# Kernel tuning notes

Measured on AMD Instinct MI355X. Metric: run time of the kernel, lower is better.

The kernel has to match this reference:

```python
import jax, jax.numpy as jnp
import numpy as np

N, E, D, L = 50000, 400000, 128, 5
NTYPE, NATTR, NDEPTH = 100, 100, 21
BN_EPS = 1e-5


def _bn(z, gamma, beta):
    # training-mode BatchNorm1d over the node axis (biased variance, as torch)
    mu = jnp.mean(z, axis=0)
    var = jnp.mean(jnp.square(z - mu), axis=0)
    return (z - mu) * jax.lax.rsqrt(var + BN_EPS) * gamma + beta


def setup_inputs() -> dict:
    key = jax.random.key(0)
    ks = jax.random.split(key, 20)
    s = 0.05
    inp = {
        "x": jax.random.randint(ks[0], (N, 2), 0, NTYPE),
        "node_depth": jax.random.randint(ks[1], (N,), 0, NDEPTH),
        "edge_index": jax.random.randint(ks[2], (2, E), 0, N),
        "edge_attr": jax.random.normal(ks[3], (E, 2), dtype=jnp.float32),
        # node encoder tables
        "type_emb": jax.random.normal(ks[4], (NTYPE, D)) * s,
        "attr_emb": jax.random.normal(ks[5], (NATTR, D)) * s,
        "depth_emb": jax.random.normal(ks[6], (NDEPTH, D)) * s,
        # per-layer GIN params, stacked over L
        "We": jax.random.normal(ks[7], (L, 2, D)) * s,
        "be": jnp.zeros((L, D)),
        "eps": jnp.zeros((L,)),
        "W1": jax.random.normal(ks[8], (L, D, 2 * D)) * s,
        "b1": jnp.zeros((L, 2 * D)),
        "g1": jnp.ones((L, 2 * D)),
        "bt1": jnp.zeros((L, 2 * D)),
        "W2": jax.random.normal(ks[9], (L, 2 * D, D)) * s,
        "b2": jnp.zeros((L, D)),
        "go": jnp.ones((L, D)),
        "bo": jnp.zeros((L, D)),
    }
    return inp


def reference(x, node_depth, edge_index, edge_attr,
              type_emb, attr_emb, depth_emb,
              We, be, eps, W1, b1, g1, bt1, W2, b2, go, bo):
    # node encoder: type + attr + depth embeddings  -> [N, D]
    h = (type_emb[x[:, 0]] + attr_emb[x[:, 1]]
         + depth_emb[jnp.clip(node_depth, 0, NDEPTH - 1)])
    src, dst = edge_index[0], edge_index[1]
    n = h.shape[0]
    for l in range(L):
        # GINConv: gather -> relu(x_j + edge_emb) -> scatter-add
        edge_emb = edge_attr @ We[l] + be[l]                 # [E, D]
        msg = jax.nn.relu(h[src] + edge_emb)                 # [E, D]
        agg = jax.ops.segment_sum(msg, dst, num_segments=n)  # [N, D]
        z = (1.0 + eps[l]) * h + agg
        # mlp: Linear -> BN -> ReLU -> Linear
        z = _bn(z @ W1[l] + b1[l], g1[l], bt1[l])
        z = jax.nn.relu(z) @ W2[l] + b2[l]
        # outer batchnorm
        z = _bn(z, go[l], bo[l])
        if l < L - 1:  # relu on all but last layer (dropout p=0 -> identity)
            z = jax.nn.relu(z)
        h = z
    return h  # JK='last'
```

## Files before the change

### kernel.cpp

```cpp
#include <hip/hip_runtime.h>
#include <hip/hip_bf16.h>

#define NN  50000
#define NE  400000
#define DD  128
#define DD2 256
#define NL  5
#define NB_SCAN 196
#define GB  256
#define NCH 1563

typedef __hip_bfloat16 bf16;
typedef __attribute__((ext_vector_type(8))) short bf16x8;
typedef __attribute__((ext_vector_type(4))) float f32x4;

__device__ __forceinline__ float b2f(bf16 v) { return __bfloat162float(v); }
__device__ __forceinline__ bool probe_bf(const void* g1) {
    return ((const unsigned*)g1)[0] == 0x3F803F80u;
}
__device__ __forceinline__ float ldp(const void* p, int i, bool bf) {
    return bf ? b2f(((const bf16*)p)[i]) : ((const float*)p)[i];
}
__device__ __forceinline__ void ldp8(const void* p, int i, bool bf, float* o) {
    if (bf) {
        union { int4 v; bf16 b[8]; } u;
        u.v = *(const int4*)((const bf16*)p + i);
#pragma unroll
        for (int j = 0; j < 8; j++) o[j] = b2f(u.b[j]);
    } else {
        float4 a = *(const float4*)((const float*)p + i);
        float4 b = *(const float4*)((const float*)p + i + 4);
        o[0]=a.x; o[1]=a.y; o[2]=a.z; o[3]=a.w;
        o[4]=b.x; o[5]=b.y; o[6]=b.z; o[7]=b.w;
    }
}

__global__ void enc_kernel(const int* __restrict__ x, const int* __restrict__ dep,
                           const void* te, const void* ae, const void* de,
                           const void* probe, float* __restrict__ h,
                           bf16* __restrict__ h2, int h2ok) {
    int t = blockIdx.x * 256 + threadIdx.x;
    if (t >= NN * DD) return;
    bool bf = probe_bf(probe);
    int i = t >> 7, d = t & (DD - 1);
    int dp = dep[i];
    dp = dp < 0 ? 0 : (dp > 20 ? 20 : dp);
    float a = ldp(te, x[2 * i] * DD + d, bf);
    float b = ldp(ae, x[2 * i + 1] * DD + d, bf);
    float c = ldp(de, dp * DD + d, bf);
    float s;
    if (bf) {
        s = b2f(__float2bfloat16(a + b));
        s = b2f(__float2bfloat16(s + c));
    } else {
        s = a + b + c;
    }
    h[t] = s;
    if (h2ok) h2[t] = __float2bfloat16(s);
}

__global__ void hist_kernel(const int* __restrict__ ei, int* __restrict__ cnt) {
    int e = blockIdx.x * 256 + threadIdx.x;
    if (e < NE) atomicAdd(&cnt[ei[NE + e]], 1);
}

__global__ void bsum_kernel(const int* __restrict__ cnt, int* __restrict__ bsum) {
    __shared__ int sm[256];
    int i = blockIdx.x * 256 + threadIdx.x;
    sm[threadIdx.x] = (i < NN) ? cnt[i] : 0;
    __syncthreads();
    for (int s = 128; s > 0; s >>= 1) {
        if (threadIdx.x < s) sm[threadIdx.x] += sm[threadIdx.x + s];
        __syncthreads();
    }
    if (threadIdx.x == 0) bsum[blockIdx.x] = sm[0];
}

__global__ void bscan_kernel(const int* __restrict__ bsum, int* __restrict__ boff, int nb) {
    __shared__ int sm[256];
    int t = threadIdx.x;
    int v = (t < nb) ? bsum[t] : 0;
    sm[t] = v; __syncthreads();
    for (int s = 1; s < 256; s <<= 1) {
        int a = (t >= s) ? sm[t - s] : 0;
        __syncthreads();
        sm[t] += a;
        __syncthreads();
    }
    if (t < nb) boff[t] = sm[t] - v;
}

__global__ void offs_kernel(const int* __restrict__ cnt, const int* __restrict__ boff,
                            int* __restrict__ offs, int* __restrict__ cur) {
    __shared__ int sm[256];
    int t = threadIdx.x;
    int i = blockIdx.x * 256 + t;
    int v = (i < NN) ? cnt[i] : 0;
    sm[t] = v; __syncthreads();
    for (int s = 1; s < 256; s <<= 1) {
        int a = (t >= s) ? sm[t - s] : 0;
        __syncthreads();
        sm[t] += a;
        __syncthreads();
    }
    int excl = sm[t] - v + boff[blockIdx.x];
    if (i < NN) { offs[i] = excl; cur[i] = excl; }
    if (i == NN - 1) offs[NN] = excl + v;
}

__global__ void place_kernel(const int* __restrict__ ei, const float* __restrict__ ea,
                             int* __restrict__ cur, int* __restrict__ srcS,
                             unsigned* __restrict__ eaS) {
    int e = blockIdx.x * 256 + threadIdx.x;
    if (e >= NE) return;
    int dst = ei[NE + e];
    int p = atomicAdd(&cur[dst], 1);
    srcS[p] = ei[e];
    union { bf16 b[2]; unsigned u; } pk;
    pk.b[0] = __float2bfloat16(ea[2 * e]);
    pk.b[1] = __float2bfloat16(ea[2 * e + 1]);
    eaS[p] = pk.u;
}

__global__ void wtrans2_kernel(const void* W1, const void* W2, const void* probe,
                               bf16* __restrict__ W1tH, bf16* __restrict__ W1tL,
                               bf16* __restrict__ W2tH, bf16* __restrict__ W2tL) {
    bool bf = probe_bf(probe);
    int idx = blockIdx.x * 256 + threadIdx.x;
    if (idx >= NL * DD * DD2) return;
    int l = idx / (DD * DD2), rem = idx % (DD * DD2);
    {
        int k = rem / DD2, n = rem % DD2;
        float w = ldp(W1, idx, bf);
        bf16 hb = __float2bfloat16(w);
        size_t o = ((size_t)l * DD2 + n) * DD + k;
        W1tH[o] = hb;
        W1tL[o] = __float2bfloat16(w - b2f(hb));
    }
    {
        int k = rem / DD, n = rem % DD;
        float w = ldp(W2, idx, bf);
        bf16 hb = __float2bfloat16(w);
        size_t o = ((size_t)l * DD + n) * DD2 + k;
        W2tH[o] = hb;
        W2tL[o] = __float2bfloat16(w - b2f(hb));
    }
}

template<int H2>
__global__ __launch_bounds__(256)
void agg_v2(const int* __restrict__ offs, const int* __restrict__ srcS,
            const unsigned* __restrict__ eaS, const void* We, const void* be,
            const void* epsp, const void* probe, const float* __restrict__ h,
            const bf16* __restrict__ h2, float* __restrict__ zpre, int l) {
    bool bf = probe_bf(probe);
    int wave = threadIdx.x >> 6, lane = threadIdx.x & 63;
    int node = blockIdx.x * 4 + wave;
    if (node >= NN) return;
    int d0 = lane * 2;
    float w00 = ldp(We, l * 2 * DD + d0, bf),      w01 = ldp(We, l * 2 * DD + d0 + 1, bf);
    float w10 = ldp(We, l * 2 * DD + DD + d0, bf), w11 = ldp(We, l * 2 * DD + DD + d0 + 1, bf);
    float bb0 = ldp(be, l * DD + d0, bf),          bb1 = ldp(be, l * DD + d0 + 1, bf);
    float cf = 1.0f + ldp(epsp, l, bf);
    int s = offs[node], e = offs[node + 1];
    float acc0 = 0.f, acc1 = 0.f;
    int j = s;
#define AGG_ONE(SRC, EA)                                                        \
    {   float hx, hy;                                                          \
        if (H2) { union { unsigned u; bf16 b[2]; } hv;                         \
                  hv.u = *(const unsigned*)&h2[(size_t)(SRC) * DD + d0];       \
                  hx = b2f(hv.b[0]); hy = b2f(hv.b[1]); }                      \
        else    { float2 hv = *(const float2*)&h[(size_t)(SRC) * DD + d0];     \
                  hx = hv.x; hy = hv.y; }                                      \
        union { unsigned u; bf16 b[2]; } ap; ap.u = (EA);                      \
        float ax = b2f(ap.b[0]), ay = b2f(ap.b[1]);                            \
        acc0 += fmaxf(hx + ax * w00 + ay * w10 + bb0, 0.f);                    \
        acc1 += fmaxf(hy + ax * w01 + ay * w11 + bb1, 0.f); }
    for (; j + 8 <= e; j += 8) {
        int i0=srcS[j],i1=srcS[j+1],i2=srcS[j+2],i3=srcS[j+3];
        int i4=srcS[j+4],i5=srcS[j+5],i6=srcS[j+6],i7=srcS[j+7];
        unsigned e0=eaS[j],e1=eaS[j+1],e2=eaS[j+2],e3=eaS[j+3];
        unsigned e4=eaS[j+4],e5=eaS[j+5],e6=eaS[j+6],e7=eaS[j+7];
        AGG_ONE(i0,e0) AGG_ONE(i1,e1) AGG_ONE(i2,e2) AGG_ONE(i3,e3)
        AGG_ONE(i4,e4) AGG_ONE(i5,e5) AGG_ONE(i6,e6) AGG_ONE(i7,e7)
    }
    for (; j + 4 <= e; j += 4) {
        int i0=srcS[j],i1=srcS[j+1],i2=srcS[j+2],i3=srcS[j+3];
        unsigned e0=eaS[j],e1=eaS[j+1],e2=eaS[j+2],e3=eaS[j+3];
        AGG_ONE(i0,e0) AGG_ONE(i1,e1) AGG_ONE(i2,e2) AGG_ONE(i3,e3)
    }
    for (; j < e; j++) { int i0 = srcS[j]; unsigned e0 = eaS[j]; AGG_ONE(i0,e0) }
#undef AGG_ONE
    float2 hs = *(const float2*)&h[(size_t)node * DD + d0];
    float2 o; o.x = fmaf(cf, hs.x, acc0); o.y = fmaf(cf, hs.y, acc1);
    *(float2*)&zpre[(size_t)node * DD + d0] = o;
}

__global__ __launch_bounds__(512, 2)
void gemm1_v2(const float* __restrict__ zpre, const bf16* __restrict__ W1tH,
              const bf16* __restrict__ W1tL, const void* b1, const void* probe,
              bf16* __restrict__ z1, float* __restrict__ P1s, float* __restrict__ P1q,
              int l) {
    __shared__ float smS[DD2], smQ[DD2];
    bool bf = probe_bf(probe);
    int tid = threadIdx.x;
    int lane = tid & 63, wave = tid >> 6;
    int wq = wave & 3, wr = wave >> 2;
    int ln15 = lane & 15, kg = lane >> 4;

    const bf16* WlH = W1tH + (size_t)l * DD2 * DD;
    const bf16* WlL = W1tL + (size_t)l * DD2 * DD;

    bf16x8 bh[4][4], bl[4][4];
#pragma unroll
    for (int t = 0; t < 4; t++) {
        int n = (wq * 4 + t) * 16 + ln15;
#pragma unroll
        for (int s = 0; s < 4; s++) {
            size_t off = (size_t)n * DD + s * 32 + kg * 8;
            bh[t][s] = *(const bf16x8*)&WlH[off];
            bl[t][s] = *(const bf16x8*)&WlL[off];
        }
    }
    float bias[4];
#pragma unroll
    for (int t = 0; t < 4; t++) bias[t] = ldp(b1, l * DD2 + (wq * 4 + t) * 16 + ln15, bf);

    float sp[4] = {0.f, 0.f, 0.f, 0.f}, qp[4] = {0.f, 0.f, 0.f, 0.f};

    for (int chunk = blockIdx.x; chunk < NCH; chunk += GB) {
        int rowbase = chunk * 32 + wr * 16;
        int arow = rowbase + ln15;
        bool aval = arow < NN;
        f32x4 acc[4];
#pragma unroll
        for (int t = 0; t < 4; t++) acc[t] = (f32x4){0.f, 0.f, 0.f, 0.f};
#pragma unroll
        for (int s = 0; s < 4; s++) {
            float av[8];
            if (aval) {
                float4 p0 = *(const float4*)&zpre[(size_t)arow * DD + s * 32 + kg * 8];
                float4 p1 = *(const float4*)&zpre[(size_t)arow * DD + s * 32 + kg * 8 + 4];
                av[0]=p0.x; av[1]=p0.y; av[2]=p0.z; av[3]=p0.w;
                av[4]=p1.x; av[5]=p1.y; av[6]=p1.z; av[7]=p1.w;
            } else {
#pragma unroll
                for (int j = 0; j < 8; j++) av[j] = 0.f;
            }
            union { bf16x8 v; bf16 e[8]; } ahi, alo;
#pragma unroll
            for (int j = 0; j < 8; j++) {
                bf16 hb = __float2bfloat16(av[j]);
                ahi.e[j] = hb;
                alo.e[j] = __float2bfloat16(av[j] - b2f(hb));
            }
#pragma unroll
            for (int t = 0; t < 4; t++) {
                acc[t] = __builtin_amdgcn_mfma_f32_16x16x32_bf16(ahi.v, bh[t][s], acc[t], 0, 0, 0);
                acc[t] = __builtin_amdgcn_mfma_f32_16x16x32_bf16(alo.v, bh[t][s], acc[t], 0, 0, 0);
                acc[t] = __builtin_amdgcn_mfma_f32_16x16x32_bf16(ahi.v, bl[t][s], acc[t], 0, 0, 0);
            }
        }
#pragma unroll
        for (int t = 0; t < 4; t++) {
            int col = (wq * 4 + t) * 16 + ln15;
#pragma unroll
            for (int r = 0; r < 4; r++) {
                int row = rowbase + kg * 4 + r;
                if (row < NN) {
                    float zv = acc[t][r] + bias[t];
                    bf16 zb = __float2bfloat16(zv);
                    z1[(size_t)row * DD2 + col] = zb;
                    float vv = b2f(zb);
                    sp[t] += vv; qp[t] += vv * vv;
                }
            }
        }
    }
#pragma unroll
    for (int t = 0; t < 4; t++) {
        sp[t] += __shfl_xor(sp[t], 16); sp[t] += __shfl_xor(sp[t], 32);
        qp[t] += __shfl_xor(qp[t], 16); qp[t] += __shfl_xor(qp[t], 32);
    }
    if (tid < DD2) { smS[tid] = 0.f; smQ[tid] = 0.f; }
    __syncthreads();
    if ((lane & 48) == 0) {
#pragma unroll
        for (int t = 0; t < 4; t++) {
            int col = (wq * 4 + t) * 16 + ln15;
            atomicAdd(&smS[col], sp[t]);
            atomicAdd(&smQ[col], qp[t]);
        }
    }
    __syncthreads();
    if (tid < DD2) {
        P1s[(size_t)blockIdx.x * DD2 + tid] = smS[tid];
        P1q[(size_t)blockIdx.x * DD2 + tid] = smQ[tid];
    }
}

__global__ __launch_bounds__(512, 2)
void gemm2_v2(const bf16* __restrict__ z1, const float* __restrict__ s1,
              const float* __restrict__ t1, const bf16* __restrict__ W2tH,
              const bf16* __restrict__ W2tL, const void* b2, const void* probe,
              float* __restrict__ out, float* __restrict__ P2s, float* __restrict__ P2q,
              int l) {
    __shared__ float smS[DD], smQ[DD];
    bool bf = probe_bf(probe);
    int tid = threadIdx.x;
    int lane = tid & 63, wave = tid >> 6;
    int wq = wave & 3, wr = wave >> 2;
    int ln15 = lane & 15, kg = lane >> 4;

    const bf16* WlH = W2tH + (size_t)l * DD * DD2;
    const bf16* WlL = W2tL + (size_t)l * DD * DD2;

    bf16x8 bh[2][8], bl[2][8];
#pragma unroll
    for (int t = 0; t < 2; t++) {
        int n = (wq * 2 + t) * 16 + ln15;
#pragma unroll
        for (int s = 0; s < 8; s++) {
            size_t off = (size_t)n * DD2 + s * 32 + kg * 8;
            bh[t][s] = *(const bf16x8*)&WlH[off];
            bl[t][s] = *(const bf16x8*)&WlL[off];
        }
    }
    float bias[2];
#pragma unroll
    for (int t = 0; t < 2; t++) bias[t] = ldp(b2, l * DD + (wq * 2 + t) * 16 + ln15, bf);

    float sp[2] = {0.f, 0.f}, qp[2] = {0.f, 0.f};

    for (int chunk = blockIdx.x; chunk < NCH; chunk += GB) {
        int rowbase = chunk * 32 + wr * 16;
        int arow = rowbase + ln15;
        bool aval = arow < NN;
        f32x4 acc[2];
        acc[0] = (f32x4){0.f, 0.f, 0.f, 0.f};
        acc[1] = (f32x4){0.f, 0.f, 0.f, 0.f};
#pragma unroll
        for (int s = 0; s < 8; s++) {
            int k0 = s * 32 + kg * 8;
            float az[8];
            if (aval) {
                union { int4 v; bf16 b[8]; } u;
                u.v = *(const int4*)&z1[(size_t)arow * DD2 + k0];
                float4 c0 = *(const float4*)&s1[k0];
                float4 c1 = *(const float4*)&s1[k0 + 4];
                float4 d0 = *(const float4*)&t1[k0];
                float4 d1 = *(const float4*)&t1[k0 + 4];
                float sc[8] = {c0.x,c0.y,c0.z,c0.w,c1.x,c1.y,c1.z,c1.w};
                float tt[8] = {d0.x,d0.y,d0.z,d0.w,d1.x,d1.y,d1.z,d1.w};
#pragma unroll
                for (int j = 0; j < 8; j++)
                    az[j] = fmaxf(fmaf(b2f(u.b[j]), sc[j], tt[j]), 0.f);
            } else {
#pragma unroll
                for (int j = 0; j < 8; j++) az[j] = 0.f;
            }
            union { bf16x8 v; bf16 e[8]; } ahi, alo;
#pragma unroll
            for (int j = 0; j < 8; j++) {
                bf16 hb = __float2bfloat16(az[j]);
                ahi.e[j] = hb;
                alo.e[j] = __float2bfloat16(az[j] - b2f(hb));
            }
#pragma unroll
            for (int t = 0; t < 2; t++) {
                acc[t] = __builtin_amdgcn_mfma_f32_16x16x32_bf16(ahi.v, bh[t][s], acc[t], 0, 0, 0);
                acc[t] = __builtin_amdgcn_mfma_f32_16x16x32_bf16(alo.v, bh[t][s], acc[t], 0, 0, 0);
                acc[t] = __builtin_amdgcn_mfma_f32_16x16x32_bf16(ahi.v, bl[t][s], acc[t], 0, 0, 0);
            }
        }
#pragma unroll
        for (int t = 0; t < 2; t++) {
            int col = (wq * 2 + t) * 16 + ln15;
#pragma unroll
            for (int r = 0; r < 4; r++) {
                int row = rowbase + kg * 4 + r;
                if (row < NN) {
                    float zv = acc[t][r] + bias[t];
                    out[(size_t)row * DD + col] = zv;
                    sp[t] += zv; qp[t] += zv * zv;
                }
            }
        }
    }
#pragma unroll
    for (int t = 0; t < 2; t++) {
        sp[t] += __shfl_xor(sp[t], 16); sp[t] += __shfl_xor(sp[t], 32);
        qp[t] += __shfl_xor(qp[t], 16); qp[t] += __shfl_xor(qp[t], 32);
    }
    if (tid < DD) { smS[tid] = 0.f; smQ[tid] = 0.f; }
    __syncthreads();
    if ((lane & 48) == 0) {
#pragma unroll
        for (int t = 0; t < 2; t++) {
            int col = (wq * 2 + t) * 16 + ln15;
            atomicAdd(&smS[col], sp[t]);
            atomicAdd(&smQ[col], qp[t]);
        }
    }
    __syncthreads();
    if (tid < DD) {
        P2s[(size_t)blockIdx.x * DD + tid] = smS[tid];
        P2q[(size_t)blockIdx.x * DD + tid] = smQ[tid];
    }
}

template<int C>
__global__ void fin_v3(const float* __restrict__ Ps, const float* __restrict__ Pq,
                       const void* gamma, const void* beta, const void* probe,
                       float* __restrict__ s, float* __restrict__ t, int l) {
    __shared__ float rs[256], rq[256];
    int c = blockIdx.x;
    int b = threadIdx.x;
    rs[b] = Ps[(size_t)b * C + c];
    rq[b] = Pq[(size_t)b * C + c];
    __syncthreads();
    for (int k = 128; k > 0; k >>= 1) {
        if (b < k) { rs[b] += rs[b + k]; rq[b] += rq[b + k]; }
        __syncthreads();
    }
    if (b == 0) {
        bool bf = probe_bf(probe);
        const float inv = 1.0f / (float)NN;
        float mu = rs[0] * inv;
        float var = rq[0] * inv - mu * mu;
        float sc = ldp(gamma, l * C + c, bf) * rsqrtf(var + 1e-5f);
        s[c] = sc;
        t[c] = ldp(beta, l * C + c, bf) - mu * sc;
    }
}

__global__ void bn_apply2(const float* __restrict__ zin, const float* __restrict__ s,
                          const float* __restrict__ t, float* __restrict__ out,
                          bf16* __restrict__ h2, int relu, int h2ok) {
    int i = blockIdx.x * 256 + threadIdx.x;
    if (i >= NN * DD / 4) return;
    int d = (i * 4) & (DD - 1);
    float4 v = ((const float4*)zin)[i];
    float4 sc = *(const float4*)&s[d];
    float4 tt = *(const float4*)&t[d];
    float4 r;
    r.x = fmaf(v.x, sc.x, tt.x);
    r.y = fmaf(v.y, sc.y, tt.y);
    r.z = fmaf(v.z, sc.z, tt.z);
    r.w = fmaf(v.w, sc.w, tt.w);
    if (relu) {
        r.x = fmaxf(r.x, 0.f); r.y = fmaxf(r.y, 0.f);
        r.z = fmaxf(r.z, 0.f); r.w = fmaxf(r.w, 0.f);
    }
    ((float4*)out)[i] = r;
    if (h2ok) {
        union { bf16 b[4]; int2 p; } o;
        o.b[0] = __float2bfloat16(r.x); o.b[1] = __float2bfloat16(r.y);
        o.b[2] = __float2bfloat16(r.z); o.b[3] = __float2bfloat16(r.w);
        *(int2*)&h2[(size_t)i * 4] = o.p;
    }
}

__global__ void scatter_kernel(const int* __restrict__ ei, const float* __restrict__ ea,
                               const void* We, const void* be, const void* probe,
                               const float* __restrict__ h, float* __restrict__ agg,
                               int l, int aok) {
    if (!aok) return;
    bool bf = probe_bf(probe);
    int e = blockIdx.x * 2 + (threadIdx.x >> 7);
    int d = threadIdx.x & (DD - 1);
    int src = ei[e];
    int dst = ei[NE + e];
    float a0 = ea[2 * e], a1 = ea[2 * e + 1];
    float w0 = ldp(We, l * 2 * DD + d, bf);
    float w1 = ldp(We, l * 2 * DD + DD + d, bf);
    float bb = ldp(be, l * DD + d, bf);
    float m = h[src * DD + d] + a0 * w0 + a1 * w1 + bb;
    if (m > 0.0f) atomicAdd(&agg[dst * DD + d], m);
}

__global__ __launch_bounds__(256)
void gemm1_kernel(const float* __restrict__ zin, const float* __restrict__ h,
                  const void* W1, const void* b1, const void* epsp, const void* probe,
                  bf16* __restrict__ z1, int l, int zok) {
    __shared__ float zs[32][36];
    __shared__ float wsh[32][DD2];
    bool bf = probe_bf(probe);
    int tid = threadIdx.x;
    int tx = tid & 31, ty = tid >> 5;
    int row0 = blockIdx.x * 32;
    if (row0 >= NN) return;
    float cf = 1.0f + ldp(epsp, l, bf);
    float acc[4][8];
#pragma unroll
    for (int i = 0; i < 4; i++)
#pragma unroll
        for (int j = 0; j < 8; j++) acc[i][j] = 0.0f;
    int lrow = tid >> 3, lkc = (tid & 7) * 4, wkr = tid >> 5, wcol = (tid & 31) * 8;
    for (int k0 = 0; k0 < DD; k0 += 32) {
        int gr = row0 + lrow;
        float4 zv = make_float4(0.f, 0.f, 0.f, 0.f);
        if (gr < NN) {
            zv = *(const float4*)&zin[gr * DD + k0 + lkc];
            float4 hv = *(const float4*)&h[gr * DD + k0 + lkc];
            zv.x = fmaf(cf, hv.x, zv.x); zv.y = fmaf(cf, hv.y, zv.y);
            zv.z = fmaf(cf, hv.z, zv.z); zv.w = fmaf(cf, hv.w, zv.w);
        }
        *(float4*)&zs[lrow][lkc] = zv;
#pragma unroll
        for (int m = 0; m < 4; m++) {
            int kr = wkr + m * 8;
            float wv[8];
            ldp8(W1, l * DD * DD2 + (k0 + kr) * DD2 + wcol, bf, wv);
            *(float4*)&wsh[kr][wcol]     = make_float4(wv[0], wv[1], wv[2], wv[3]);
            *(float4*)&wsh[kr][wcol + 4] = make_float4(wv[4], wv[5], wv[6], wv[7]);
        }
        __syncthreads();
#pragma unroll 4
        for (int kk = 0; kk < 32; kk++) {
            float zr[4];
#pragma unroll
            for (int i = 0; i < 4; i++) zr[i] = zs[ty * 4 + i][kk];
            float4 w0 = *(float4*)&wsh[kk][tx * 8];
            float4 w1 = *(float4*)&wsh[kk][tx * 8 + 4];
            float wv[8] = {w0.x, w0.y, w0.z, w0.w, w1.x, w1.y, w1.z, w1.w};
#pragma unroll
            for (int i = 0; i < 4; i++)
#pragma unroll
                for (int j = 0; j < 8; j++)
                    acc[i][j] = fmaf(zr[i], wv[j], acc[i][j]);
        }
        __syncthreads();
    }
    float bv[8];
    ldp8(b1, l * DD2 + tx * 8, bf, bv);
#pragma unroll
    for (int i = 0; i < 4; i++) {
        int gr = row0 + ty * 4 + i;
        if (gr < NN && zok) {
            union { int4 v; bf16 b[8]; } o;
#pragma unroll
            for (int j = 0; j < 8; j++) o.b[j] = __float2bfloat16(acc[i][j] + bv[j]);
            *(int4*)&z1[(long)gr * DD2 + tx * 8] = o.v;
        }
    }
}

__global__ __launch_bounds__(256)
void gemm2_kernel(const bf16* __restrict__ z1, const float* __restrict__ s1,
                  const float* __restrict__ t1, const void* W2, const void* b2,
                  const void* probe, float* __restrict__ out, int l, int aok, int zok) {
    __shared__ float zs[32][36];
    __shared__ float wsh[32][DD];
    bool bf = probe_bf(probe);
    int tid = threadIdx.x;
    int tx = tid & 15, ty = tid >> 4;
    int row0 = blockIdx.x * 32;
    if (row0 >= NN) return;
    float acc[2][8];
#pragma unroll
    for (int i = 0; i < 2; i++)
#pragma unroll
        for (int j = 0; j < 8; j++) acc[i][j] = 0.0f;
    int lrow = tid >> 3, lkc = (tid & 7) * 4, wkr = tid >> 4, wcol = (tid & 15) * 8;
    for (int k0 = 0; k0 < DD2; k0 += 32) {
        int gr = row0 + lrow;
        float4 zv = make_float4(0.f, 0.f, 0.f, 0.f);
        if (gr < NN && zok) {
            union { int2 v; bf16 b[4]; } u;
            u.v = *(const int2*)&z1[(long)gr * DD2 + k0 + lkc];
            float4 sc = *(const float4*)&s1[k0 + lkc];
            float4 tt = *(const float4*)&t1[k0 + lkc];
            zv.x = fmaxf(0.f, fmaf(b2f(u.b[0]), sc.x, tt.x));
            zv.y = fmaxf(0.f, fmaf(b2f(u.b[1]), sc.y, tt.y));
            zv.z = fmaxf(0.f, fmaf(b2f(u.b[2]), sc.z, tt.z));
            zv.w = fmaxf(0.f, fmaf(b2f(u.b[3]), sc.w, tt.w));
        }
        *(float4*)&zs[lrow][lkc] = zv;
#pragma unroll
        for (int m = 0; m < 2; m++) {
            int kr = wkr + m * 16;
            float wv[8];
            ldp8(W2, l * DD2 * DD + (k0 + kr) * DD + wcol, bf, wv);
            *(float4*)&wsh[kr][wcol]     = make_float4(wv[0], wv[1], wv[2], wv[3]);
            *(float4*)&wsh[kr][wcol + 4] = make_float4(wv[4], wv[5], wv[6], wv[7]);
        }
        __syncthreads();
#pragma unroll 4
        for (int kk = 0; kk < 32; kk++) {
            float zr[2];
            zr[0] = zs[ty * 2][kk];
            zr[1] = zs[ty * 2 + 1][kk];
            float4 w0 = *(float4*)&wsh[kk][tx * 8];
            float4 w1 = *(float4*)&wsh[kk][tx * 8 + 4];
            float wv[8] = {w0.x, w0.y, w0.z, w0.w, w1.x, w1.y, w1.z, w1.w};
#pragma unroll
            for (int i = 0; i < 2; i++)
#pragma unroll
                for (int j = 0; j < 8; j++)
                    acc[i][j] = fmaf(zr[i], wv[j], acc[i][j]);
        }
        __syncthreads();
    }
    float bv[8];
    ldp8(b2, l * DD + tx * 8, bf, bv);
#pragma unroll
    for (int i = 0; i < 2; i++) {
        int gr = row0 + ty * 2 + i;
        if (gr < NN && aok) {
            float4 o0 = make_float4(acc[i][0] + bv[0], acc[i][1] + bv[1],
                                    acc[i][2] + bv[2], acc[i][3] + bv[3]);
            float4 o1 = make_float4(acc[i][4] + bv[4], acc[i][5] + bv[5],
                                    acc[i][6] + bv[6], acc[i][7] + bv[7]);
            *(float4*)&out[gr * DD + tx * 8] = o0;
            *(float4*)&out[gr * DD + tx * 8 + 4] = o1;
        }
    }
}

__global__ void bn_stats1_kernel(const bf16* __restrict__ z, float* __restrict__ sum,
                                 float* __restrict__ sq, int zok) {
    int col = threadIdx.x;
    int rbase = blockIdx.x * 256;
    int rend = rbase + 256; if (rend > NN) rend = NN;
    float s = 0.0f, q = 0.0f;
    if (zok)
        for (int r = rbase; r < rend; r++) {
            float v = b2f(z[(long)r * DD2 + col]);
            s += v; q += v * v;
        }
    atomicAdd(&sum[col], s);
    atomicAdd(&sq[col], q);
}

__global__ void bn_stats2_kernel(const float* __restrict__ z, float* __restrict__ sum,
                                 float* __restrict__ sq, int aok) {
    int col = threadIdx.x & (DD - 1);
    int roff = threadIdx.x >> 7;
    int rbase = blockIdx.x * 256;
    int rend = rbase + 256; if (rend > NN) rend = NN;
    float s = 0.0f, q = 0.0f;
    if (aok)
        for (int r = rbase + roff; r < rend; r += 2) {
            float v = z[(long)r * DD + col];
            s += v; q += v * v;
        }
    atomicAdd(&sum[col], s);
    atomicAdd(&sq[col], q);
}

template<int C>
__global__ void bn_finalize_kernel(const float* __restrict__ sum, const float* __restrict__ sq,
                                   const void* gamma, const void* beta, const void* probe,
                                   float* __restrict__ s, float* __restrict__ t, int l) {
    int c = threadIdx.x;
    if (c >= C) return;
    bool bf = probe_bf(probe);
    const float inv = 1.0f / (float)NN;
    float mu = sum[c] * inv;
    float var = sq[c] * inv - mu * mu;
    float sc = ldp(gamma, l * C + c, bf) * rsqrtf(var + 1e-5f);
    s[c] = sc;
    t[c] = ldp(beta, l * C + c, bf) - mu * sc;
}

extern "C" void kernel_launch(void* const* d_in, const int* in_sizes, int n_in,
                              void* d_out, int out_size, void* d_ws, size_t ws_size,
                              hipStream_t stream) {
    const int*   x   = (const int*)d_in[0];
    const int*   dep = (const int*)d_in[1];
    const int*   ei  = (const int*)d_in[2];
    const float* ea  = (const float*)d_in[3];
    const void* te  = d_in[4];
    const void* ae  = d_in[5];
    const void* de  = d_in[6];
    const void* We  = d_in[7];
    const void* be  = d_in[8];
    const void* eps = d_in[9];
    const void* W1  = d_in[10];
    const void* b1  = d_in[11];
    const void* g1  = d_in[12];
    const void* bt1 = d_in[13];
    const void* W2  = d_in[14];
    const void* b2  = d_in[15];
    const void* go  = d_in[16];
    const void* bo  = d_in[17];

    float* h  = (float*)d_out;
    float* ws = (float*)d_ws;
    float* sum1 = ws;
    float* sq1  = ws + 256;
    float* sum2 = ws + 512;
    float* sq2  = ws + 640;
    float* s1   = ws + 768;
    float* t1   = ws + 1024;
    float* s2   = ws + 1280;
    float* t2   = ws + 1408;

    float*  P1s  = ws + 2048;
    float*  P1q  = P1s + GB * DD2;
    float*  P2s  = P1q + GB * DD2;
    float*  P2q  = P2s + GB * DD;
    int*    cnt  = (int*)(P2q + GB * DD);
    int*    offs = cnt + 50048;
    int*    cur  = offs + 50048;
    int*    bsum = cur + 50048;
    int*    boff = bsum + 256;
    int*    srcS = boff + 256;
    unsigned* eaS = (unsigned*)(srcS + NE);
    float*  zpreS = (float*)(eaS + NE);
    bf16*   z1S   = (bf16*)(zpreS + (size_t)NN * DD);
    bf16*   W1tH  = z1S + (size_t)NN * DD2;
    bf16*   W1tL  = W1tH + (size_t)NL * DD2 * DD;
    bf16*   W2tH  = W1tL + (size_t)NL * DD2 * DD;
    bf16*   W2tL  = W2tH + (size_t)NL * DD * DD2;
    bf16*   h2    = W2tL + (size_t)NL * DD * DD2;
    size_t need_noh2 = (size_t)((char*)h2 - (char*)d_ws);
    size_t need_full = need_noh2 + (size_t)NN * DD * sizeof(bf16);

    float* zpreF = ws + 2048;
    bf16*  z1F   = (bf16*)(zpreF + (size_t)NN * DD);
    size_t need_a = 2048u * 4 + (size_t)NN * DD * 4;
    size_t need_z = need_a + (size_t)NN * DD2 * 2;

    int mode = ws_size >= need_full ? 2 : (ws_size >= need_noh2 ? 1 : 0);
    int aok = mode || ws_size >= need_a ? 1 : 0;
    int zok = mode || ws_size >= need_z ? 1 : 0;
    float* zpre = mode ? zpreS : zpreF;
    bf16*  z1   = mode ? z1S   : z1F;

    enc_kernel<<<(NN * DD + 255) / 256, 256, 0, stream>>>(x, dep, te, ae, de, g1, h, h2, mode == 2);

    if (mode) {
        hipMemsetAsync(cnt, 0, 50048 * sizeof(int), stream);
        hist_kernel<<<(NE + 255) / 256, 256, 0, stream>>>(ei, cnt);
        bsum_kernel<<<NB_SCAN, 256, 0, stream>>>(cnt, bsum);
        bscan_kernel<<<1, 256, 0, stream>>>(bsum, boff, NB_SCAN);
        offs_kernel<<<NB_SCAN, 256, 0, stream>>>(cnt, boff, offs, cur);
        place_kernel<<<(NE + 255) / 256, 256, 0, stream>>>(ei, ea, cur, srcS, eaS);
        wtrans2_kernel<<<(NL * DD * DD2 + 255) / 256, 256, 0, stream>>>(W1, W2, g1, W1tH, W1tL, W2tH, W2tL);
    }

    for (int l = 0; l < NL; l++) {
        if (mode) {
            if (mode == 2)
                agg_v2<1><<<(NN + 3) / 4, 256, 0, stream>>>(offs, srcS, eaS, We, be, eps, g1, h, h2, zpre, l);
            else
                agg_v2<0><<<(NN + 3) / 4, 256, 0, stream>>>(offs, srcS, eaS, We, be, eps, g1, h, h2, zpre, l);
            gemm1_v2<<<GB, 512, 0, stream>>>(zpre, W1tH, W1tL, b1, g1, z1, P1s, P1q, l);
            fin_v3<DD2><<<DD2, 256, 0, stream>>>(P1s, P1q, g1, bt1, g1, s1, t1, l);
            gemm2_v2<<<GB, 512, 0, stream>>>(z1, s1, t1, W2tH, W2tL, b2, g1, zpre, P2s, P2q, l);
            fin_v3<DD><<<DD, 256, 0, stream>>>(P2s, P2q, go, bo, g1, s2, t2, l);
            bn_apply2<<<(NN * DD / 4 + 255) / 256, 256, 0, stream>>>(
                zpre, s2, t2, h, h2, l < NL - 1 ? 1 : 0, (mode == 2 && l < NL - 1) ? 1 : 0);
        } else {
            hipMemsetAsync(ws, 0, 768 * sizeof(float), stream);
            if (aok) hipMemsetAsync(zpre, 0, (size_t)NN * DD * sizeof(float), stream);
            scatter_kernel<<<NE / 2, 256, 0, stream>>>(ei, ea, We, be, g1, h, zpre, l, aok);
            gemm1_kernel<<<(NN + 31) / 32, 256, 0, stream>>>(zpre, h, W1, b1, eps, g1, z1, l, zok);
            bn_stats1_kernel<<<(NN + 255) / 256, 256, 0, stream>>>(z1, sum1, sq1, zok);
            bn_finalize_kernel<DD2><<<1, DD2, 0, stream>>>(sum1, sq1, g1, bt1, g1, s1, t1, l);
            gemm2_kernel<<<(NN + 31) / 32, 256, 0, stream>>>(z1, s1, t1, W2, b2, g1, zpre, l, aok, zok);
            bn_stats2_kernel<<<(NN + 255) / 256, 256, 0, stream>>>(zpre, sum2, sq2, aok);
            bn_finalize_kernel<DD><<<1, DD, 0, stream>>>(sum2, sq2, go, bo, g1, s2, t2, l);
            bn_apply2<<<(NN * DD / 4 + 255) / 256, 256, 0, stream>>>(
                zpre, s2, t2, h, h2, l < NL - 1 ? 1 : 0, 0);
        }
    }
}
```

Measured before the change: 668.5 us.

## Fuse outer BatchNorm apply into next layer's aggregation and gemm2 epilogue

Drops the per-layer bn_apply2 pass. gemm2 now writes the pre-BN output, plus a bf16 shadow copy, directly into the buffer that holds the next layer's input. The next agg kernel then applies the BN scale, shift and ReLU on the fly to each gathered neighbour row and to its own row. A single bn_apply2 runs after the last layer. This removes a full read and write of the N×D activations per layer. In exchange the affine+ReLU is recomputed once per edge gather, and the bf16 shadow now stores pre-BN values, which changes how rounding interacts with the normalization.

Measured after the change: 642.9 us (median of 2 runs). -3.8%, faster.

```diff
diff --git a/kernel.cpp b/kernel.cpp
--- a/kernel.cpp
+++ b/kernel.cpp
@@ -147,12 +147,13 @@
     }
 }
 
-template<int H2>
+template<int H2, int FIRST>
 __global__ __launch_bounds__(256)
-void agg_v2(const int* __restrict__ offs, const int* __restrict__ srcS,
+void agg_v3(const int* __restrict__ offs, const int* __restrict__ srcS,
             const unsigned* __restrict__ eaS, const void* We, const void* be,
-            const void* epsp, const void* probe, const float* __restrict__ h,
-            const bf16* __restrict__ h2, float* __restrict__ zpre, int l) {
+            const void* epsp, const void* probe, const float* __restrict__ zmid,
+            const bf16* __restrict__ zmid2, const float* __restrict__ s2v,
+            const float* __restrict__ t2v, float* __restrict__ aggout, int l) {
     bool bf = probe_bf(probe);
     int wave = threadIdx.x >> 6, lane = threadIdx.x & 63;
     int node = blockIdx.x * 4 + wave;
@@ -162,16 +163,26 @@
     float w10 = ldp(We, l * 2 * DD + DD + d0, bf), w11 = ldp(We, l * 2 * DD + DD + d0 + 1, bf);
     float bb0 = ldp(be, l * DD + d0, bf),          bb1 = ldp(be, l * DD + d0 + 1, bf);
     float cf = 1.0f + ldp(epsp, l, bf);
+    float s20 = 1.f, s21 = 1.f, t20 = 0.f, t21 = 0.f;
+    if (!FIRST) {
+        float2 sv = *(const float2*)&s2v[d0];
+        float2 tv = *(const float2*)&t2v[d0];
+        s20 = sv.x; s21 = sv.y; t20 = tv.x; t21 = tv.y;
+    }
     int s = offs[node], e = offs[node + 1];
     float acc0 = 0.f, acc1 = 0.f;
     int j = s;
 #define AGG_ONE(SRC, EA)                                                        \
     {   float hx, hy;                                                          \
         if (H2) { union { unsigned u; bf16 b[2]; } hv;                         \
-                  hv.u = *(const unsigned*)&h2[(size_t)(SRC) * DD + d0];       \
+                  hv.u = *(const unsigned*)&zmid2[(size_t)(SRC) * DD + d0];    \
                   hx = b2f(hv.b[0]); hy = b2f(hv.b[1]); }                      \
-        else    { float2 hv = *(const float2*)&h[(size_t)(SRC) * DD + d0];     \
+        else    { float2 hv = *(const float2*)&zmid[(size_t)(SRC) * DD + d0];  \
                   hx = hv.x; hy = hv.y; }                                      \
+        if (!FIRST) {                                                          \
+            hx = fmaxf(fmaf(hx, s20, t20), 0.f);                               \
+            hy = fmaxf(fmaf(hy, s21, t21), 0.f);                               \
+        }                                                                      \
         union { unsigned u; bf16 b[2]; } ap; ap.u = (EA);                      \
         float ax = b2f(ap.b[0]), ay = b2f(ap.b[1]);                            \
         acc0 += fmaxf(hx + ax * w00 + ay * w10 + bb0, 0.f);                    \
@@ -191,9 +202,14 @@
     }
     for (; j < e; j++) { int i0 = srcS[j]; unsigned e0 = eaS[j]; AGG_ONE(i0,e0) }
 #undef AGG_ONE
-    float2 hs = *(const float2*)&h[(size_t)node * DD + d0];
-    float2 o; o.x = fmaf(cf, hs.x, acc0); o.y = fmaf(cf, hs.y, acc1);
-    *(float2*)&zpre[(size_t)node * DD + d0] = o;
+    float2 zs = *(const float2*)&zmid[(size_t)node * DD + d0];
+    float h0 = zs.x, h1 = zs.y;
+    if (!FIRST) {
+        h0 = fmaxf(fmaf(h0, s20, t20), 0.f);
+        h1 = fmaxf(fmaf(h1, s21, t21), 0.f);
+    }
+    float2 o; o.x = fmaf(cf, h0, acc0); o.y = fmaf(cf, h1, acc1);
+    *(float2*)&aggout[(size_t)node * DD + d0] = o;
 }
 
 __global__ __launch_bounds__(512, 2)
@@ -303,8 +319,8 @@
 void gemm2_v2(const bf16* __restrict__ z1, const float* __restrict__ s1,
               const float* __restrict__ t1, const bf16* __restrict__ W2tH,
               const bf16* __restrict__ W2tL, const void* b2, const void* probe,
-              float* __restrict__ out, float* __restrict__ P2s, float* __restrict__ P2q,
-              int l) {
+              float* __restrict__ out, bf16* __restrict__ out2, int shadow,
+              float* __restrict__ P2s, float* __restrict__ P2q, int l) {
     __shared__ float smS[DD], smQ[DD];
     bool bf = probe_bf(probe);
     int tid = threadIdx.x;
@@ -382,6 +398,7 @@
                 if (row < NN) {
                     float zv = acc[t][r] + bias[t];
                     out[(size_t)row * DD + col] = zv;
+                    if (shadow) out2[(size_t)row * DD + col] = __float2bfloat16(zv);
                     sp[t] += zv; qp[t] += zv * zv;
                 }
             }
@@ -686,7 +703,7 @@
     const void* go  = d_in[16];
     const void* bo  = d_in[17];
 
-    float* h  = (float*)d_out;
+    float* zmid = (float*)d_out;
     float* ws = (float*)d_ws;
     float* sum1 = ws;
     float* sq1  = ws + 256;
@@ -708,14 +725,14 @@
     int*    boff = bsum + 256;
     int*    srcS = boff + 256;
     unsigned* eaS = (unsigned*)(srcS + NE);
-    float*  zpreS = (float*)(eaS + NE);
-    bf16*   z1S   = (bf16*)(zpreS + (size_t)NN * DD);
+    float*  aggout = (float*)(eaS + NE);
+    bf16*   z1S   = (bf16*)(aggout + (size_t)NN * DD);
     bf16*   W1tH  = z1S + (size_t)NN * DD2;
     bf16*   W1tL  = W1tH + (size_t)NL * DD2 * DD;
     bf16*   W2tH  = W1tL + (size_t)NL * DD2 * DD;
     bf16*   W2tL  = W2tH + (size_t)NL * DD * DD2;
-    bf16*   h2    = W2tL + (size_t)NL * DD * DD2;
-    size_t need_noh2 = (size_t)((char*)h2 - (char*)d_ws);
+    bf16*   zmid2 = W2tL + (size_t)NL * DD * DD2;
+    size_t need_noh2 = (size_t)((char*)zmid2 - (char*)d_ws);
     size_t need_full = need_noh2 + (size_t)NN * DD * sizeof(bf16);
 
     float* zpreF = ws + 2048;
@@ -726,10 +743,9 @@
     int mode = ws_size >= need_full ? 2 : (ws_size >= need_noh2 ? 1 : 0);
     int aok = mode || ws_size >= need_a ? 1 : 0;
     int zok = mode || ws_size >= need_z ? 1 : 0;
-    float* zpre = mode ? zpreS : zpreF;
-    bf16*  z1   = mode ? z1S   : z1F;
-
-    enc_kernel<<<(NN * DD + 255) / 256, 256, 0, stream>>>(x, dep, te, ae, de, g1, h, h2, mode == 2);
+    bf16* z1 = mode ? z1S : z1F;
+
+    enc_kernel<<<(NN * DD + 255) / 256, 256, 0, stream>>>(x, dep, te, ae, de, g1, zmid, zmid2, mode == 2);
 
     if (mode) {
         hipMemsetAsync(cnt, 0, 50048 * sizeof(int), stream);
@@ -743,28 +759,40 @@
 
     for (int l = 0; l < NL; l++) {
         if (mode) {
-            if (mode == 2)
-                agg_v2<1><<<(NN + 3) / 4, 256, 0, stream>>>(offs, srcS, eaS, We, be, eps, g1, h, h2, zpre, l);
-            else
-                agg_v2<0><<<(NN + 3) / 4, 256, 0, stream>>>(offs, srcS, eaS, We, be, eps, g1, h, h2, zpre, l);
-            gemm1_v2<<<GB, 512, 0, stream>>>(zpre, W1tH, W1tL, b1, g1, z1, P1s, P1q, l);
+            if (mode == 2) {
+                if (l == 0)
+                    agg_v3<1,1><<<(NN + 3) / 4, 256, 0, stream>>>(offs, srcS, eaS, We, be, eps, g1,
+                                                                  zmid, zmid2, s2, t2, aggout, l);
+                else
+                    agg_v3<1,0><<<(NN + 3) / 4, 256, 0, stream>>>(offs, srcS, eaS, We, be, eps, g1,
+                                                                  zmid, zmid2, s2, t2, aggout, l);
+            } else {
+                if (l == 0)
+                    agg_v3<0,1><<<(NN + 3) / 4, 256, 0, stream>>>(offs, srcS, eaS, We, be, eps, g1,
+                                                                  zmid, zmid2, s2, t2, aggout, l);
+                else
+                    agg_v3<0,0><<<(NN + 3) / 4, 256, 0, stream>>>(offs, srcS, eaS, We, be, eps, g1,
+                                                                  zmid, zmid2, s2, t2, aggout, l);
+            }
+            gemm1_v2<<<GB, 512, 0, stream>>>(aggout, W1tH, W1tL, b1, g1, z1, P1s, P1q, l);
             fin_v3<DD2><<<DD2, 256, 0, stream>>>(P1s, P1q, g1, bt1, g1, s1, t1, l);
-            gemm2_v2<<<GB, 512, 0, stream>>>(z1, s1, t1, W2tH, W2tL, b2, g1, zpre, P2s, P2q, l);
+            gemm2_v2<<<GB, 512, 0, stream>>>(z1, s1, t1, W2tH, W2tL, b2, g1, zmid, zmid2,
+                                             (mode == 2 && l < NL - 1) ? 1 : 0, P2s, P2q, l);
             fin_v3<DD><<<DD, 256, 0, stream>>>(P2s, P2q, go, bo, g1, s2, t2, l);
-            bn_apply2<<<(NN * DD / 4 + 255) / 256, 256, 0, stream>>>(
-                zpre, s2, t2, h, h2, l < NL - 1 ? 1 : 0, (mode == 2 && l < NL - 1) ? 1 : 0);
         } else {
             hipMemsetAsync(ws, 0, 768 * sizeof(float), stream);
-            if (aok) hipMemsetAsync(zpre, 0, (size_t)NN * DD * sizeof(float), stream);
-            scatter_kernel<<<NE / 2, 256, 0, stream>>>(ei, ea, We, be, g1, h, zpre, l, aok);
-            gemm1_kernel<<<(NN + 31) / 32, 256, 0, stream>>>(zpre, h, W1, b1, eps, g1, z1, l, zok);
+            if (aok) hipMemsetAsync(zpreF, 0, (size_t)NN * DD * sizeof(float), stream);
+            scatter_kernel<<<NE / 2, 256, 0, stream>>>(ei, ea, We, be, g1, zmid, zpreF, l, aok);
+            gemm1_kernel<<<(NN + 31) / 32, 256, 0, stream>>>(zpreF, zmid, W1, b1, eps, g1, z1, l, zok);
             bn_stats1_kernel<<<(NN + 255) / 256, 256, 0, stream>>>(z1, sum1, sq1, zok);
             bn_finalize_kernel<DD2><<<1, DD2, 0, stream>>>(sum1, sq1, g1, bt1, g1, s1, t1, l);
-            gemm2_kernel<<<(NN + 31) / 32, 256, 0, stream>>>(z1, s1, t1, W2, b2, g1, zpre, l, aok, zok);
-            bn_stats2_kernel<<<(NN + 255) / 256, 256, 0, stream>>>(zpre, sum2, sq2, aok);
+            gemm2_kernel<<<(NN + 31) / 32, 256, 0, stream>>>(z1, s1, t1, W2, b2, g1, zpreF, l, aok, zok);
+            bn_stats2_kernel<<<(NN + 255) / 256, 256, 0, stream>>>(zpreF, sum2, sq2, aok);
             bn_finalize_kernel<DD><<<1, DD, 0, stream>>>(sum2, sq2, go, bo, g1, s2, t2, l);
             bn_apply2<<<(NN * DD / 4 + 255) / 256, 256, 0, stream>>>(
-                zpre, s2, t2, h, h2, l < NL - 1 ? 1 : 0, 0);
-        }
-    }
-}
+                zpreF, s2, t2, zmid, zmid2, l < NL - 1 ? 1 : 0, 0);
+        }
+    }
+    if (mode)
+        bn_apply2<<<(NN * DD / 4 + 255) / 256, 256, 0, stream>>>(zmid, s2, t2, zmid, zmid2, 0, 0);
+}
```
